# Kernel tuning notes

Hardware: AMD Instinct MI355X
Metric: run time of the kernel (lower is better)

The kernel has to match this reference:

```python
import jax, jax.numpy as jnp
import numpy as np

N, C, F, T = 8, 4, 257, 2000
B = 8            # spatial_filters (beams)
M = 80           # spectra_filters
EPS = 1e-5


def setup_inputs() -> dict:
    key = jax.random.key(0)
    ks = jax.random.split(key, 10)
    scale = 0.1
    return {
        "x_real": jax.random.normal(ks[0], (N, C, F, T), jnp.float32),
        "x_imag": jax.random.normal(ks[1], (N, C, F, T), jnp.float32),
        # query beamformer (1 beam): conv weights per bin, shape (F, 1, C)
        "wq_r": jax.random.normal(ks[2], (F, 1, C), jnp.float32) * scale,
        "wq_i": jax.random.normal(ks[3], (F, 1, C), jnp.float32) * scale,
        # key/value beamformers: (F, B, C)
        "wk_r": jax.random.normal(ks[4], (F, B, C), jnp.float32) * scale,
        "wk_i": jax.random.normal(ks[5], (F, B, C), jnp.float32) * scale,
        "wv_r": jax.random.normal(ks[6], (F, B, C), jnp.float32) * scale,
        "wv_i": jax.random.normal(ks[7], (F, B, C), jnp.float32) * scale,
        # spectra projection Linear(F -> M, bias=False): torch weight (M, F)
        "proj_w": jax.random.normal(ks[8], (M, F), jnp.float32) * (1.0 / np.sqrt(F)),
        # BatchNorm1d(M) affine params
        "bn_gamma": jnp.ones((M,), jnp.float32),
        "bn_beta": jnp.zeros((M,), jnp.float32),
    }


def _complex_beam_abs(xr, xi, wr, wi):
    # xr/xi: (N,T,F,C); wr/wi: (F,Beams,C)
    # grouped per-bin conv with kernel==length reduces to contraction over C
    rr = jnp.einsum("ntfc,fbc->ntfb", xr, wr)
    ii = jnp.einsum("ntfc,fbc->ntfb", xi, wi)
    ri = jnp.einsum("ntfc,fbc->ntfb", xi, wr)
    ir = jnp.einsum("ntfc,fbc->ntfb", xr, wi)
    br = rr - ii
    bi = ri + ir
    return jnp.sqrt(br * br + bi * bi + EPS)


def reference(x_real, x_imag, wq_r, wq_i, wk_r, wk_i, wv_r, wv_i, proj_w, bn_gamma, bn_beta):
    # N,C,F,T -> N,T,F,C
    xr = jnp.transpose(x_real, (0, 3, 2, 1))
    xi = jnp.transpose(x_imag, (0, 3, 2, 1))
    bq = _complex_beam_abs(xr, xi, wq_r, wq_i)[..., 0]   # (N,T,F)
    bk = _complex_beam_abs(xr, xi, wk_r, wk_i)           # (N,T,F,B)
    bv = _complex_beam_abs(xr, xi, wv_r, wv_i)           # (N,T,F,B)
    s = jnp.sum(bq[..., None] * bk, axis=-2)             # (N,T,B)
    s = jnp.mean(s, axis=-2, keepdims=True)              # (N,1,B) time-invariant
    w = jax.nn.softmax(s, axis=-1)                       # (N,1,B)
    v = jnp.sum(w[:, None] * bv, axis=-1)                # (N,T,F)
    f = jax.nn.relu(jnp.einsum("ntf,mf->ntm", v, proj_w))
    f = jnp.log(f + EPS)                                 # (N,T,M)
    # BatchNorm1d over channel dim M, training-mode batch stats (biased var)
    mu = jnp.mean(f, axis=(0, 1))
    var = jnp.var(f, axis=(0, 1))
    f = (f - mu) * jax.lax.rsqrt(var + EPS) * bn_gamma + bn_beta
    return f
```

## Files before the change

kernel.cpp:

```cpp
#include <hip/hip_runtime.h>
#include <math.h>

#define NN 8
#define CC 4
#define FF 257
#define TT 2000
#define BB 8
#define MM 80
#define EPSF 1e-5f
#define VSTR 260
#define T4N 500

typedef float v2f __attribute__((ext_vector_type(2)));

__device__ __forceinline__ float fsqrt_fast(float x) { return __builtin_amdgcn_sqrtf(x); }
__device__ __forceinline__ float flog_fast(float x)  { return __builtin_amdgcn_logf(x) * 0.69314718055994531f; }
__device__ __forceinline__ v2f sqrt2(v2f m) {
    v2f r; r.x = __builtin_amdgcn_sqrtf(m.x); r.y = __builtin_amdgcn_sqrtf(m.y); return r;
}

__global__ __launch_bounds__(256) void k_beam_s(
    const float* __restrict__ xr_g, const float* __restrict__ xi_g,
    const float* __restrict__ wq_r, const float* __restrict__ wq_i,
    const float* __restrict__ wk_r, const float* __restrict__ wk_i,
    float* __restrict__ s_buf)
{
    int nf = blockIdx.x;
    int n = nf / FF, f = nf % FF;
    int t4 = blockIdx.y * 256 + threadIdx.x;

    float part[BB];
#pragma unroll
    for (int b = 0; b < BB; ++b) part[b] = 0.f;

    if (t4 < T4N) {
        const float* xr_base = xr_g + ((size_t)(n*CC)*FF + f) * TT + t4*4;
        const float* xi_base = xi_g + ((size_t)(n*CC)*FF + f) * TT + t4*4;
        v2f xr2[CC][2], xi2[CC][2];
#pragma unroll
        for (int c = 0; c < CC; ++c) {
            float4 r4 = *reinterpret_cast<const float4*>(xr_base + (size_t)c*FF*TT);
            float4 i4 = *reinterpret_cast<const float4*>(xi_base + (size_t)c*FF*TT);
            xr2[c][0].x = r4.x; xr2[c][0].y = r4.y; xr2[c][1].x = r4.z; xr2[c][1].y = r4.w;
            xi2[c][0].x = i4.x; xi2[c][0].y = i4.y; xi2[c][1].x = i4.z; xi2[c][1].y = i4.w;
        }

        const float4 qr4 = *reinterpret_cast<const float4*>(&wq_r[f*CC]);
        const float4 qi4 = *reinterpret_cast<const float4*>(&wq_i[f*CC]);

        v2f qq[2];
#pragma unroll
        for (int p = 0; p < 2; ++p) {
            v2f qr = xr2[0][p]*qr4.x + xr2[1][p]*qr4.y + xr2[2][p]*qr4.z + xr2[3][p]*qr4.w
                   - xi2[0][p]*qi4.x - xi2[1][p]*qi4.y - xi2[2][p]*qi4.z - xi2[3][p]*qi4.w;
            v2f qi = xi2[0][p]*qr4.x + xi2[1][p]*qr4.y + xi2[2][p]*qr4.z + xi2[3][p]*qr4.w
                   + xr2[0][p]*qi4.x + xr2[1][p]*qi4.y + xr2[2][p]*qi4.z + xr2[3][p]*qi4.w;
            qq[p] = qr*qr + qi*qi + EPSF;
        }

#pragma unroll
        for (int b = 0; b < BB; ++b) {
            const float4 wr4 = *reinterpret_cast<const float4*>(&wk_r[(f*BB + b)*CC]);
            const float4 wi4 = *reinterpret_cast<const float4*>(&wk_i[(f*BB + b)*CC]);
            v2f acc; acc.x = 0.f; acc.y = 0.f;
#pragma unroll
            for (int p = 0; p < 2; ++p) {
                v2f kr = xr2[0][p]*wr4.x + xr2[1][p]*wr4.y + xr2[2][p]*wr4.z + xr2[3][p]*wr4.w
                       - xi2[0][p]*wi4.x - xi2[1][p]*wi4.y - xi2[2][p]*wi4.z - xi2[3][p]*wi4.w;
                v2f ki = xi2[0][p]*wr4.x + xi2[1][p]*wr4.y + xi2[2][p]*wr4.z + xi2[3][p]*wr4.w
                       + xr2[0][p]*wi4.x + xr2[1][p]*wi4.y + xr2[2][p]*wi4.z + xr2[3][p]*wi4.w;
                v2f kk = kr*kr + ki*ki + EPSF;
                acc += sqrt2(qq[p] * kk);
            }
            part[b] = acc.x + acc.y;
        }
    }

    __shared__ float red[4][BB];
    int lane = threadIdx.x & 63, wv = threadIdx.x >> 6;
#pragma unroll
    for (int b = 0; b < BB; ++b) {
        float v = part[b];
#pragma unroll
        for (int m = 32; m >= 1; m >>= 1) v += __shfl_xor(v, m);
        if (lane == 0) red[wv][b] = v;
    }
    __syncthreads();
    if (threadIdx.x < BB) {
        float v = red[0][threadIdx.x] + red[1][threadIdx.x]
                + red[2][threadIdx.x] + red[3][threadIdx.x];
        int bin = (blockIdx.x * 2 + blockIdx.y) & 15;
        atomicAdd(&s_buf[bin*64 + n*BB + threadIdx.x], v);
    }
}

__global__ void k_softmax(const float* __restrict__ s_buf, float* __restrict__ w_buf)
{
    int tid = threadIdx.x;
    if (tid < NN*BB) {
        float v = 0.f;
#pragma unroll
        for (int j = 0; j < 16; ++j) v += s_buf[j*64 + tid];
        v *= (1.0f / TT);
        float mx = v;
#pragma unroll
        for (int m = 4; m >= 1; m >>= 1) mx = fmaxf(mx, __shfl_xor(mx, m));
        float e = expf(v - mx);
        float sm = e;
#pragma unroll
        for (int m = 4; m >= 1; m >>= 1) sm += __shfl_xor(sm, m);
        w_buf[tid] = e / sm;
    }
}

__global__ void k_prep(const float* __restrict__ proj_w, float* __restrict__ proj_pad)
{
    int i = blockIdx.x * 256 + threadIdx.x;
    if (i < MM * 260) {
        int m = i / 260, f = i % 260;
        proj_pad[i] = (f < FF) ? proj_w[m*FF + f] : 0.f;
    }
}

__global__ __launch_bounds__(256, 4) void k_vproj(
    const float* __restrict__ xr_g, const float* __restrict__ xi_g,
    const float* __restrict__ wv_r, const float* __restrict__ wv_i,
    const float* __restrict__ w_buf, const float* __restrict__ proj_pad,
    float* __restrict__ out, double* __restrict__ bn_sum, double* __restrict__ bn_sumsq)
{
    __shared__ float v_lds[16 * VSTR];
    int n = blockIdx.x, chunk = blockIdx.y;
    int t0 = chunk * 16;
    int tid = threadIdx.x;

    float wn[BB];
#pragma unroll
    for (int b = 0; b < BB; ++b) wn[b] = w_buf[n*BB + b];

    if (tid < 64 && (tid & 3) < 3) {
        int t = tid >> 2, f = FF + (tid & 3);
        v_lds[t*VSTR + f] = 0.f;
    }

    if (tid < 16) {
        int t = t0 + tid;
        float xr[CC], xi[CC];
#pragma unroll
        for (int c = 0; c < CC; ++c) {
            size_t base = ((size_t)(n*CC + c)*FF + 256)*TT + t;
            xr[c] = xr_g[base];
            xi[c] = xi_g[base];
        }
        float v = 0.f;
#pragma unroll
        for (int b = 0; b < BB; ++b) {
            const float4 wr4 = *reinterpret_cast<const float4*>(&wv_r[(256*BB + b)*CC]);
            const float4 wi4 = *reinterpret_cast<const float4*>(&wv_i[(256*BB + b)*CC]);
            float vr = xr[0]*wr4.x + xr[1]*wr4.y + xr[2]*wr4.z + xr[3]*wr4.w
                     - xi[0]*wi4.x - xi[1]*wi4.y - xi[2]*wi4.z - xi[3]*wi4.w;
            float vi = xi[0]*wr4.x + xi[1]*wr4.y + xi[2]*wr4.z + xi[3]*wr4.w
                     + xr[0]*wi4.x + xr[1]*wi4.y + xr[2]*wi4.z + xr[3]*wi4.w;
            v += wn[b] * fsqrt_fast(vr*vr + vi*vi + EPSF);
        }
        v_lds[tid*VSTR + 256] = v;
    }

    int t4s = tid & 3;
    int fbase = tid >> 2;

#pragma unroll 2
    for (int k = 0; k < 4; ++k) {
        int f = fbase + 64*k;
        v2f xr2[CC][2], xi2[CC][2];
#pragma unroll
        for (int c = 0; c < CC; ++c) {
            size_t base = ((size_t)(n*CC + c)*FF + f)*TT + t0 + t4s*4;
            float4 r4 = *reinterpret_cast<const float4*>(xr_g + base);
            float4 i4 = *reinterpret_cast<const float4*>(xi_g + base);
            xr2[c][0].x = r4.x; xr2[c][0].y = r4.y; xr2[c][1].x = r4.z; xr2[c][1].y = r4.w;
            xi2[c][0].x = i4.x; xi2[c][0].y = i4.y; xi2[c][1].x = i4.z; xi2[c][1].y = i4.w;
        }

        v2f vo[2];
        vo[0].x = 0.f; vo[0].y = 0.f; vo[1].x = 0.f; vo[1].y = 0.f;
#pragma unroll
        for (int b = 0; b < BB; ++b) {
            const float4 wr4 = *reinterpret_cast<const float4*>(&wv_r[(f*BB + b)*CC]);
            const float4 wi4 = *reinterpret_cast<const float4*>(&wv_i[(f*BB + b)*CC]);
#pragma unroll
            for (int p = 0; p < 2; ++p) {
                v2f vr = xr2[0][p]*wr4.x + xr2[1][p]*wr4.y + xr2[2][p]*wr4.z + xr2[3][p]*wr4.w
                       - xi2[0][p]*wi4.x - xi2[1][p]*wi4.y - xi2[2][p]*wi4.z - xi2[3][p]*wi4.w;
                v2f vi = xi2[0][p]*wr4.x + xi2[1][p]*wr4.y + xi2[2][p]*wr4.z + xi2[3][p]*wr4.w
                       + xr2[0][p]*wi4.x + xr2[1][p]*wi4.y + xr2[2][p]*wi4.z + xr2[3][p]*wi4.w;
                vo[p] += wn[b] * sqrt2(vr*vr + vi*vi + EPSF);
            }
        }
        v_lds[(t4s*4 + 0)*VSTR + f] = vo[0].x;
        v_lds[(t4s*4 + 1)*VSTR + f] = vo[0].y;
        v_lds[(t4s*4 + 2)*VSTR + f] = vo[1].x;
        v_lds[(t4s*4 + 3)*VSTR + f] = vo[1].y;
    }
    __syncthreads();

    int tl = tid & 15, fg = tid >> 4;
    v2f acc2[5];
#pragma unroll
    for (int j = 0; j < 5; ++j) { acc2[j].x = 0.f; acc2[j].y = 0.f; }
    const float* pp = proj_pad + fg * 5 * 260;
#pragma unroll 4
    for (int f4 = 0; f4 < 260; f4 += 4) {
        float4 vv = *reinterpret_cast<const float4*>(&v_lds[tl*VSTR + f4]);
        v2f v0, v1;
        v0.x = vv.x; v0.y = vv.y; v1.x = vv.z; v1.y = vv.w;
#pragma unroll
        for (int j = 0; j < 5; ++j) {
            float4 p = *reinterpret_cast<const float4*>(&pp[j*260 + f4]);
            v2f p0, p1; p0.x = p.x; p0.y = p.y; p1.x = p.z; p1.y = p.w;
            acc2[j] += v0*p0 + v1*p1;
        }
    }

    int t = t0 + tl;
    int bin = chunk & 15;
#pragma unroll
    for (int j = 0; j < 5; ++j) {
        int m = fg*5 + j;
        float r = flog_fast(fmaxf(acc2[j].x + acc2[j].y, 0.f) + EPSF);
        float s1 = r, s2 = r*r;
#pragma unroll
        for (int msk = 8; msk >= 1; msk >>= 1) {
            s1 += __shfl_xor(s1, msk);
            s2 += __shfl_xor(s2, msk);
        }
        out[((size_t)n*TT + t)*MM + m] = r;
        if (tl == 0) {
            atomicAdd(&bn_sum[bin*MM + m], (double)s1);
            atomicAdd(&bn_sumsq[bin*MM + m], (double)s2);
        }
    }
}

__global__ void k_bnprep(const double* __restrict__ bn_sum, const double* __restrict__ bn_sumsq,
                         const float* __restrict__ gamma, const float* __restrict__ beta,
                         float* __restrict__ scale, float* __restrict__ shift)
{
    int m = threadIdx.x;
    if (m < MM) {
        double s = 0.0, q = 0.0;
#pragma unroll
        for (int j = 0; j < 16; ++j) { s += bn_sum[j*MM + m]; q += bn_sumsq[j*MM + m]; }
        double inv = 1.0 / (double)(NN * TT);
        double mu = s * inv;
        double var = q * inv - mu * mu;
        float sc = gamma[m] * rsqrtf((float)var + EPSF);
        scale[m] = sc;
        shift[m] = beta[m] - (float)mu * sc;
    }
}

__global__ __launch_bounds__(256) void k_bnapply(float* __restrict__ out,
                                                 const float* __restrict__ scale,
                                                 const float* __restrict__ shift)
{
    int i4 = blockIdx.x * 256 + threadIdx.x;
    if (i4 < NN*TT*MM/4) {
        float4 v = *reinterpret_cast<const float4*>(&out[i4*4]);
        int m = (i4*4) % MM;
        v.x = v.x*scale[m+0] + shift[m+0];
        v.y = v.y*scale[m+1] + shift[m+1];
        v.z = v.z*scale[m+2] + shift[m+2];
        v.w = v.w*scale[m+3] + shift[m+3];
        *reinterpret_cast<float4*>(&out[i4*4]) = v;
    }
}

extern "C" void kernel_launch(void* const* d_in, const int* in_sizes, int n_in,
                              void* d_out, int out_size, void* d_ws, size_t ws_size,
                              hipStream_t stream)
{
    const float* x_real   = (const float*)d_in[0];
    const float* x_imag   = (const float*)d_in[1];
    const float* wq_r     = (const float*)d_in[2];
    const float* wq_i     = (const float*)d_in[3];
    const float* wk_r     = (const float*)d_in[4];
    const float* wk_i     = (const float*)d_in[5];
    const float* wv_r     = (const float*)d_in[6];
    const float* wv_i     = (const float*)d_in[7];
    const float* proj_w   = (const float*)d_in[8];
    const float* bn_gamma = (const float*)d_in[9];
    const float* bn_beta  = (const float*)d_in[10];
    float* out = (float*)d_out;

    char* ws = (char*)d_ws;
    float*  s_buf    = (float*)(ws + 0);
    float*  w_buf    = (float*)(ws + 4096);
    float*  scale    = (float*)(ws + 4352);
    float*  shift    = (float*)(ws + 4672);
    double* bn_sum   = (double*)(ws + 8192);
    double* bn_sumsq = (double*)(ws + 18432);
    float*  proj_pad = (float*)(ws + 28672);

    hipMemsetAsync(d_ws, 0, 28672, stream);

    k_prep<<<(MM*260 + 255)/256, 256, 0, stream>>>(proj_w, proj_pad);

    dim3 g1(NN*FF, 2);
    k_beam_s<<<g1, 256, 0, stream>>>(x_real, x_imag, wq_r, wq_i, wk_r, wk_i, s_buf);

    k_softmax<<<1, 64, 0, stream>>>(s_buf, w_buf);

    dim3 g3(NN, 125);
    k_vproj<<<g3, 256, 0, stream>>>(x_real, x_imag, wv_r, wv_i, w_buf, proj_pad,
                                    out, bn_sum, bn_sumsq);

    k_bnprep<<<1, 128, 0, stream>>>(bn_sum, bn_sumsq, bn_gamma, bn_beta, scale, shift);

    k_bnapply<<<(NN*TT*MM/4 + 255)/256, 256, 0, stream>>>(out, scale, shift);
}
```

Measured before the change: 110.5 us.

## Halve time tile in k_vproj and remap threads to one bin each

The value-projection kernel now processes 8 time steps per block instead of 16, doubling the grid to 250 chunks per batch item. Each thread handles one frequency bin across all 8 times, using two contiguous float4 loads per channel. The projection stage splits the 80 outputs into uneven 3/2 groups per thread pair. The intent is more blocks for occupancy and less register pressure per thread, at the cost of more blocks, more BN atomics and a divergent branch in the projection loop.

```diff
diff --git a/kernel.cpp b/kernel.cpp
--- a/kernel.cpp
+++ b/kernel.cpp
@@ -10,6 +10,8 @@
 #define EPSF 1e-5f
 #define VSTR 260
 #define T4N 500
+#define TTILE 8
+#define NCHUNK 250
 
 typedef float v2f __attribute__((ext_vector_type(2)));
 
@@ -128,21 +130,21 @@
     const float* __restrict__ w_buf, const float* __restrict__ proj_pad,
     float* __restrict__ out, double* __restrict__ bn_sum, double* __restrict__ bn_sumsq)
 {
-    __shared__ float v_lds[16 * VSTR];
+    __shared__ float v_lds[TTILE * VSTR];
     int n = blockIdx.x, chunk = blockIdx.y;
-    int t0 = chunk * 16;
+    int t0 = chunk * TTILE;
     int tid = threadIdx.x;
 
     float wn[BB];
 #pragma unroll
     for (int b = 0; b < BB; ++b) wn[b] = w_buf[n*BB + b];
 
-    if (tid < 64 && (tid & 3) < 3) {
-        int t = tid >> 2, f = FF + (tid & 3);
-        v_lds[t*VSTR + f] = 0.f;
-    }
-
-    if (tid < 16) {
+    if (tid < TTILE*3) {
+        int t = tid / 3, fp = FF + tid % 3;
+        v_lds[t*VSTR + fp] = 0.f;
+    }
+
+    if (tid < TTILE) {
         int t = t0 + tid;
         float xr[CC], xi[CC];
 #pragma unroll
@@ -165,71 +167,92 @@
         v_lds[tid*VSTR + 256] = v;
     }
 
-    int t4s = tid & 3;
-    int fbase = tid >> 2;
+    {
+        int f = tid;
+        v2f xr2[CC][4], xi2[CC][4];
+#pragma unroll
+        for (int c = 0; c < CC; ++c) {
+            size_t base = ((size_t)(n*CC + c)*FF + f)*TT + t0;
+            float4 a = *reinterpret_cast<const float4*>(xr_g + base);
+            float4 b4 = *reinterpret_cast<const float4*>(xr_g + base + 4);
+            float4 d = *reinterpret_cast<const float4*>(xi_g + base);
+            float4 e = *reinterpret_cast<const float4*>(xi_g + base + 4);
+            xr2[c][0].x = a.x;  xr2[c][0].y = a.y;
+            xr2[c][1].x = a.z;  xr2[c][1].y = a.w;
+            xr2[c][2].x = b4.x; xr2[c][2].y = b4.y;
+            xr2[c][3].x = b4.z; xr2[c][3].y = b4.w;
+            xi2[c][0].x = d.x;  xi2[c][0].y = d.y;
+            xi2[c][1].x = d.z;  xi2[c][1].y = d.w;
+            xi2[c][2].x = e.x;  xi2[c][2].y = e.y;
+            xi2[c][3].x = e.z;  xi2[c][3].y = e.w;
+        }
+
+        v2f vo[4];
+#pragma unroll
+        for (int p = 0; p < 4; ++p) { vo[p].x = 0.f; vo[p].y = 0.f; }
 
 #pragma unroll 2
-    for (int k = 0; k < 4; ++k) {
-        int f = fbase + 64*k;
-        v2f xr2[CC][2], xi2[CC][2];
-#pragma unroll
-        for (int c = 0; c < CC; ++c) {
-            size_t base = ((size_t)(n*CC + c)*FF + f)*TT + t0 + t4s*4;
-            float4 r4 = *reinterpret_cast<const float4*>(xr_g + base);
-            float4 i4 = *reinterpret_cast<const float4*>(xi_g + base);
-            xr2[c][0].x = r4.x; xr2[c][0].y = r4.y; xr2[c][1].x = r4.z; xr2[c][1].y = r4.w;
-            xi2[c][0].x = i4.x; xi2[c][0].y = i4.y; xi2[c][1].x = i4.z; xi2[c][1].y = i4.w;
-        }
-
-        v2f vo[2];
-        vo[0].x = 0.f; vo[0].y = 0.f; vo[1].x = 0.f; vo[1].y = 0.f;
-#pragma unroll
         for (int b = 0; b < BB; ++b) {
             const float4 wr4 = *reinterpret_cast<const float4*>(&wv_r[(f*BB + b)*CC]);
             const float4 wi4 = *reinterpret_cast<const float4*>(&wv_i[(f*BB + b)*CC]);
-#pragma unroll
-            for (int p = 0; p < 2; ++p) {
+            float wnb = wn[b];
+#pragma unroll
+            for (int p = 0; p < 4; ++p) {
                 v2f vr = xr2[0][p]*wr4.x + xr2[1][p]*wr4.y + xr2[2][p]*wr4.z + xr2[3][p]*wr4.w
                        - xi2[0][p]*wi4.x - xi2[1][p]*wi4.y - xi2[2][p]*wi4.z - xi2[3][p]*wi4.w;
                 v2f vi = xi2[0][p]*wr4.x + xi2[1][p]*wr4.y + xi2[2][p]*wr4.z + xi2[3][p]*wr4.w
                        + xr2[0][p]*wi4.x + xr2[1][p]*wi4.y + xr2[2][p]*wi4.z + xr2[3][p]*wi4.w;
-                vo[p] += wn[b] * sqrt2(vr*vr + vi*vi + EPSF);
+                vo[p] += wnb * sqrt2(vr*vr + vi*vi + EPSF);
             }
         }
-        v_lds[(t4s*4 + 0)*VSTR + f] = vo[0].x;
-        v_lds[(t4s*4 + 1)*VSTR + f] = vo[0].y;
-        v_lds[(t4s*4 + 2)*VSTR + f] = vo[1].x;
-        v_lds[(t4s*4 + 3)*VSTR + f] = vo[1].y;
+#pragma unroll
+        for (int p = 0; p < 4; ++p) {
+            v_lds[(2*p + 0)*VSTR + f] = vo[p].x;
+            v_lds[(2*p + 1)*VSTR + f] = vo[p].y;
+        }
     }
     __syncthreads();
 
-    int tl = tid & 15, fg = tid >> 4;
-    v2f acc2[5];
-#pragma unroll
-    for (int j = 0; j < 5; ++j) { acc2[j].x = 0.f; acc2[j].y = 0.f; }
-    const float* pp = proj_pad + fg * 5 * 260;
+    int tl = tid & 7, fg = tid >> 3;
+    int mstart = (fg >> 1)*5 + ((fg & 1) ? 3 : 0);
+    bool three = !(fg & 1);
+    v2f a0, a1, a2;
+    a0.x = 0.f; a0.y = 0.f; a1.x = 0.f; a1.y = 0.f; a2.x = 0.f; a2.y = 0.f;
+    const float* pp = proj_pad + mstart*260;
 #pragma unroll 4
     for (int f4 = 0; f4 < 260; f4 += 4) {
         float4 vv = *reinterpret_cast<const float4*>(&v_lds[tl*VSTR + f4]);
         v2f v0, v1;
         v0.x = vv.x; v0.y = vv.y; v1.x = vv.z; v1.y = vv.w;
-#pragma unroll
-        for (int j = 0; j < 5; ++j) {
-            float4 p = *reinterpret_cast<const float4*>(&pp[j*260 + f4]);
-            v2f p0, p1; p0.x = p.x; p0.y = p.y; p1.x = p.z; p1.y = p.w;
-            acc2[j] += v0*p0 + v1*p1;
+        float4 p0 = *reinterpret_cast<const float4*>(&pp[f4]);
+        float4 p1 = *reinterpret_cast<const float4*>(&pp[260 + f4]);
+        {
+            v2f q0, q1; q0.x = p0.x; q0.y = p0.y; q1.x = p0.z; q1.y = p0.w;
+            a0 += v0*q0 + v1*q1;
+        }
+        {
+            v2f q0, q1; q0.x = p1.x; q0.y = p1.y; q1.x = p1.z; q1.y = p1.w;
+            a1 += v0*q0 + v1*q1;
+        }
+        if (three) {
+            float4 p2 = *reinterpret_cast<const float4*>(&pp[520 + f4]);
+            v2f q0, q1; q0.x = p2.x; q0.y = p2.y; q1.x = p2.z; q1.y = p2.w;
+            a2 += v0*q0 + v1*q1;
         }
     }
 
     int t = t0 + tl;
     int bin = chunk & 15;
-#pragma unroll
-    for (int j = 0; j < 5; ++j) {
-        int m = fg*5 + j;
-        float r = flog_fast(fmaxf(acc2[j].x + acc2[j].y, 0.f) + EPSF);
+    float accs[3];
+    accs[0] = a0.x + a0.y; accs[1] = a1.x + a1.y; accs[2] = a2.x + a2.y;
+#pragma unroll
+    for (int j = 0; j < 3; ++j) {
+        if (j == 2 && !three) break;
+        int m = mstart + j;
+        float r = flog_fast(fmaxf(accs[j], 0.f) + EPSF);
         float s1 = r, s2 = r*r;
 #pragma unroll
-        for (int msk = 8; msk >= 1; msk >>= 1) {
+        for (int msk = 4; msk >= 1; msk >>= 1) {
             s1 += __shfl_xor(s1, msk);
             s2 += __shfl_xor(s2, msk);
         }
@@ -310,7 +333,7 @@
 
     k_softmax<<<1, 64, 0, stream>>>(s_buf, w_buf);
 
-    dim3 g3(NN, 125);
+    dim3 g3(NN, NCHUNK);
     k_vproj<<<g3, 256, 0, stream>>>(x_real, x_imag, wv_r, wv_i, w_buf, proj_pad,
                                     out, bn_sum, bn_sumsq);
 
```

Result: slower. 139.2 us (+26.1%).
